# Kernel optimization log

Measured on AMD Instinct MI355X. Metric: run time of the kernel, lower is better.

Reference implementation:

```python
import jax, jax.numpy as jnp
import numpy as np

N, E, G = 50000, 800000, 64          # nodes, edges, graphs
IN, HID, OUT, H = 256, 64, 64, 4     # input dim, per-head hidden, output dim, heads
NEG_SLOPE = 0.2                      # PyG GATConv leaky_relu slope


def _lin(k, fan_in, fan_out):
    return jax.random.normal(k, (fan_in, fan_out), jnp.float32) * (1.0 / np.sqrt(fan_in))


def setup_inputs() -> dict:
    key = jax.random.key(0)
    ks = jax.random.split(key, 16)
    x = jax.random.normal(ks[0], (N, IN), jnp.float32)
    edge_index = jax.random.randint(ks[1], (2, E), 0, N, dtype=jnp.int32)
    batch = jnp.sort(jax.random.randint(ks[2], (N,), 0, G, dtype=jnp.int32))
    # layer 1: IN -> H x HID (concat)
    W1 = _lin(ks[3], IN, H * HID)
    a_src1 = jax.random.normal(ks[4], (H, HID), jnp.float32) * 0.1
    a_dst1 = jax.random.normal(ks[5], (H, HID), jnp.float32) * 0.1
    b1 = jnp.zeros((H * HID,), jnp.float32)
    # layer 2: H*HID -> H x HID (concat)
    W2 = _lin(ks[6], H * HID, H * HID)
    a_src2 = jax.random.normal(ks[7], (H, HID), jnp.float32) * 0.1
    a_dst2 = jax.random.normal(ks[8], (H, HID), jnp.float32) * 0.1
    b2 = jnp.zeros((H * HID,), jnp.float32)
    W3 = _lin(ks[9], H * HID, OUT)
    a_src3 = jax.random.normal(ks[10], (1, OUT), jnp.float32) * 0.1
    a_dst3 = jax.random.normal(ks[11], (1, OUT), jnp.float32) * 0.1
    b3 = jnp.zeros((OUT,), jnp.float32)
    return {"x": x, "edge_index": edge_index, "batch": batch,
            "W1": W1, "a_src1": a_src1, "a_dst1": a_dst1, "b1": b1,
            "W2": W2, "a_src2": a_src2, "a_dst2": a_dst2, "b2": b2,
            "W3": W3, "a_src3": a_src3, "a_dst3": a_dst3, "b3": b3}


def gat_conv(x, src, dst, W, a_src, a_dst, b, heads, out_ch):
    """PyG-style GATConv (eval mode, concat=True semantics; heads=1 == no concat)."""
    n = x.shape[0]
    h = (x @ W).reshape(n, heads, out_ch)                     # [N,H,C]
    alpha_s = jnp.sum(h * a_src, axis=-1)                     # [N,H]
    alpha_d = jnp.sum(h * a_dst, axis=-1)                     # [N,H]
    e = jax.nn.leaky_relu(alpha_s[src] + alpha_d[dst], NEG_SLOPE)  # [E',H]
    # segment softmax over destination nodes (self-loops guarantee nonempty segments)
    m = jax.ops.segment_max(e, dst, num_segments=n)
    e = jnp.exp(e - m[dst])
    denom = jax.ops.segment_sum(e, dst, num_segments=n)
    alpha = e / (denom[dst] + 1e-16)                          # [E',H]
    msg = h[src] * alpha[:, :, None]                          # [E',H,C]
    out = jax.ops.segment_sum(msg, dst, num_segments=n)       # [N,H,C]
    return out.reshape(n, heads * out_ch) + b


def reference(x, edge_index, batch, W1, a_src1, a_dst1, b1, W2, a_src2, a_dst2, b2,
              W3, a_src3, a_dst3, b3):
    n = x.shape[0]
    # GATConv default add_self_loops=True
    loops = jnp.arange(n, dtype=edge_index.dtype)
    src = jnp.concatenate([edge_index[0], loops])
    dst = jnp.concatenate([edge_index[1], loops])

    h = gat_conv(x, src, dst, W1, a_src1, a_dst1, b1, H, HID)
    h = jax.nn.elu(h)  # dropout disabled in eval
    h = gat_conv(h, src, dst, W2, a_src2, a_dst2, b2, H, HID)
    h = jax.nn.elu(h)
    node_embeddings = gat_conv(h, src, dst, W3, a_src3, a_dst3, b3, 1, OUT)

    # global_mean_pool over batch ids
    sums = jax.ops.segment_sum(node_embeddings, batch, num_segments=G)
    counts = jax.ops.segment_sum(jnp.ones((n,), node_embeddings.dtype), batch, num_segments=G)
    graph_embeddings = sums / jnp.maximum(counts, 1.0)[:, None]
    return node_embeddings, graph_embeddings
```

## Files before the change

kernel.cpp:

```cpp
#include <hip/hip_runtime.h>
#include <hip/hip_bf16.h>
#include <hip/hip_fp16.h>

typedef __attribute__((ext_vector_type(8))) _Float16 f16x8;
typedef __attribute__((ext_vector_type(4))) _Float16 f16x4;
typedef __attribute__((ext_vector_type(4))) float f32x4;

static __device__ __forceinline__ void st(float* p, float v)  { *p = v; }
static __device__ __forceinline__ void st(__half* p, float v) { *p = __float2half(v); }

static __device__ __forceinline__ void splitf16(float v, __half& hi, __half& lo) {
    hi = __float2half(v);
    lo = __float2half(v - __half2float(hi));
}

__global__ void k_pre(const int* __restrict__ ei, int* __restrict__ deg, int* __restrict__ rnk,
                      int E,
                      const float* __restrict__ x, __half* __restrict__ xh,
                      __half* __restrict__ xl, long n4,
                      const float* __restrict__ W1, const float* __restrict__ W2,
                      const float* __restrict__ W3,
                      __half* __restrict__ w1h, __half* __restrict__ w1l,
                      __half* __restrict__ w2h, __half* __restrict__ w2l,
                      __half* __restrict__ w3h, __half* __restrict__ w3l) {
    int bx = blockIdx.x;
    int nhist = (E + 255) >> 8;
    if (bx < nhist) {
        int e = bx * 256 + threadIdx.x;
        if (e < E) rnk[e] = atomicAdd(&deg[ei[E + e]], 1);
        return;
    }
    bx -= nhist;
    int nx4 = (int)((n4 + 255) >> 8);
    if (bx < nx4) {
        long i = (long)bx * 256 + threadIdx.x;
        if (i < n4) {
            float4 v = *reinterpret_cast<const float4*>(x + i * 4);
            __half h0, h1, h2, h3, l0, l1, l2, l3;
            splitf16(v.x, h0, l0);
            splitf16(v.y, h1, l1);
            splitf16(v.z, h2, l2);
            splitf16(v.w, h3, l3);
            ushort4 hv = { __half_as_ushort(h0), __half_as_ushort(h1),
                           __half_as_ushort(h2), __half_as_ushort(h3) };
            ushort4 lv = { __half_as_ushort(l0), __half_as_ushort(l1),
                           __half_as_ushort(l2), __half_as_ushort(l3) };
            *reinterpret_cast<ushort4*>(xh + i * 4) = hv;
            *reinterpret_cast<ushort4*>(xl + i * 4) = lv;
        }
        return;
    }
    bx -= nx4;
    int idx = bx * 256 + threadIdx.x;
    const float* W; __half *Wh, *Wl; int M, base;
    constexpr int K = 256;
    if (idx < 65536)       { W = W1; Wh = w1h; Wl = w1l; M = 256; base = idx; }
    else if (idx < 131072) { W = W2; Wh = w2h; Wl = w2l; M = 256; base = idx - 65536; }
    else if (idx < 147456) { W = W3; Wh = w3h; Wl = w3l; M = 64;  base = idx - 131072; }
    else return;
    int k = base / M, n = base - k * M;
    __half h, l;
    splitf16(W[base], h, l);
    Wh[(size_t)n * K + k] = h;
    Wl[(size_t)n * K + k] = l;
}

__global__ void k_scan1(const int* __restrict__ deg, int* __restrict__ offs,
                        int* __restrict__ bsum, int N) {
    __shared__ int sh[256];
    int i = blockIdx.x * 256 + threadIdx.x;
    int v = (i < N) ? (deg[i] + 1) : 0;
    sh[threadIdx.x] = v;
    __syncthreads();
#pragma unroll
    for (int off = 1; off < 256; off <<= 1) {
        int t = (threadIdx.x >= off) ? sh[threadIdx.x - off] : 0;
        __syncthreads();
        sh[threadIdx.x] += t;
        __syncthreads();
    }
    if (i < N) offs[i] = sh[threadIdx.x] - v;
    if (threadIdx.x == 255) bsum[blockIdx.x] = sh[255];
}

__global__ void k_scan2(int* __restrict__ bsum, int nb) {
    __shared__ int sh[256];
    int v = (threadIdx.x < nb) ? bsum[threadIdx.x] : 0;
    sh[threadIdx.x] = v;
    __syncthreads();
#pragma unroll
    for (int off = 1; off < 256; off <<= 1) {
        int t = (threadIdx.x >= off) ? sh[threadIdx.x - off] : 0;
        __syncthreads();
        sh[threadIdx.x] += t;
        __syncthreads();
    }
    if (threadIdx.x < nb) bsum[threadIdx.x] = sh[threadIdx.x] - v;
    if (threadIdx.x == 255) bsum[nb] = sh[255];
}

__global__ void k_scan3(int* __restrict__ offs, const int* __restrict__ deg,
                        int* __restrict__ csr, const int* __restrict__ bsum,
                        int N, int nb) {
    int i = blockIdx.x * 256 + threadIdx.x;
    if (i < N) {
        int v = offs[i] + bsum[blockIdx.x];
        offs[i] = v;
        csr[v + deg[i]] = i;
    }
    if (i == 0) offs[N] = bsum[nb];
}

template <typename ACC>
static __device__ __forceinline__ void alpha_epilogue(
        const ACC& acc, float* ldsf, const float* __restrict__ a_src,
        const float* __restrict__ a_dst, float* __restrict__ als,
        float* __restrict__ ald, __half* __restrict__ C,
        int nrows, int M, int H, int r0, int c0,
        int wr, int wc, int quad, int r, int tid) {
    float ps[4][4], pd[4][4];
#pragma unroll
    for (int tr = 0; tr < 4; ++tr)
#pragma unroll
        for (int i = 0; i < 4; ++i) { ps[tr][i] = 0.f; pd[tr][i] = 0.f; }

#pragma unroll
    for (int tr = 0; tr < 4; ++tr)
#pragma unroll
        for (int tc = 0; tc < 2; ++tc) {
            int col = c0 + wc * 32 + tc * 16 + r;
            float av_s = a_src[col], av_d = a_dst[col];
#pragma unroll
            for (int i = 0; i < 4; ++i) {
                int row = r0 + wr * 64 + tr * 16 + quad * 4 + i;
                __half hv = __float2half(acc[tr][tc][i]);
                float vr = __half2float(hv);
                if (row < nrows) C[(size_t)row * M + col] = hv;
                ps[tr][i] = fmaf(vr, av_s, ps[tr][i]);
                pd[tr][i] = fmaf(vr, av_d, pd[tr][i]);
            }
        }
#pragma unroll
    for (int tr = 0; tr < 4; ++tr)
#pragma unroll
        for (int i = 0; i < 4; ++i) {
            float s = ps[tr][i], d2 = pd[tr][i];
#pragma unroll
            for (int off = 1; off < 16; off <<= 1) {
                s  += __shfl_xor(s,  off, 64);
                d2 += __shfl_xor(d2, off, 64);
            }
            if (r == 0) {
                int lrow = wr * 64 + tr * 16 + quad * 4 + i;
                ldsf[(0 * 2 + wc) * 128 + lrow] = s;
                ldsf[(2 + wc) * 128 + lrow]     = d2;
            }
        }
    __syncthreads();
    int lrow = tid >> 1, which = tid & 1;
    if (lrow < 128) {
        float v = ldsf[(which * 2 + 0) * 128 + lrow] + ldsf[(which * 2 + 1) * 128 + lrow];
        int grow = r0 + lrow;
        if (grow < nrows) {
            float* dst = which ? ald : als;
            dst[(size_t)grow * H + (c0 >> 6)] = v;
        }
    }
}

__global__ __launch_bounds__(256) void k_g3s(const __half* __restrict__ Ah, const __half* __restrict__ Al,
                                             const __half* __restrict__ Wth, const __half* __restrict__ Wtl,
                                             __half* __restrict__ C, int nrows, int K, int M,
                                             const float* __restrict__ a_src, const float* __restrict__ a_dst,
                                             float* __restrict__ als, float* __restrict__ ald, int H,
                                             int gridRows, int gemmBlocks,
                                             const int* __restrict__ ei, const int* __restrict__ rnk,
                                             const int* __restrict__ offs, int* __restrict__ csr, int E) {
    constexpr int LDA = 40;
    __shared__ __half AH[128 * LDA];
    __shared__ __half AL[128 * LDA];
    __shared__ __half BH[64 * LDA];
    __shared__ __half BL[64 * LDA];

    int gx = blockIdx.x;
    int g = gx / 3, rsel = gx - g * 3;
    if (rsel != 0) {
        int e = (g * 2 + (rsel - 1)) * 256 + threadIdx.x;
        if (e < E) {
            int dn = ei[E + e];
            csr[offs[dn] + rnk[e]] = ei[e];
        }
        return;
    }
    if (g >= gemmBlocks) return;
    int bxg = g % gridRows, byg = g / gridRows;

    int tid  = threadIdx.x;
    int lane = tid & 63;
    int wave = tid >> 6;
    int wr = wave & 1, wc = wave >> 1;
    int quad = lane >> 4, r = lane & 15;
    int r0 = bxg * 128, c0 = byg * 64;

    f32x4 acc[4][2];
#pragma unroll
    for (int i = 0; i < 4; ++i)
#pragma unroll
        for (int j = 0; j < 2; ++j) acc[i][j] = (f32x4){0.f, 0.f, 0.f, 0.f};

    for (int kc = 0; kc < K; kc += 32) {
#pragma unroll
        for (int it = 0; it < 2; ++it) {
            int row  = (tid >> 2) + it * 64;
            int kseg = (tid & 3) * 8;
            int gr = r0 + row;
            f16x8 vh = (f16x8)(_Float16)0, vl = (f16x8)(_Float16)0;
            if (gr < nrows) {
                vh = *reinterpret_cast<const f16x8*>(Ah + (size_t)gr * K + kc + kseg);
                vl = *reinterpret_cast<const f16x8*>(Al + (size_t)gr * K + kc + kseg);
            }
            *reinterpret_cast<f16x8*>(&AH[row * LDA + kseg]) = vh;
            *reinterpret_cast<f16x8*>(&AL[row * LDA + kseg]) = vl;
        }
        {
            int n    = tid >> 2;
            int kseg = (tid & 3) * 8;
            *reinterpret_cast<f16x8*>(&BH[n * LDA + kseg]) =
                *reinterpret_cast<const f16x8*>(Wth + (size_t)(c0 + n) * K + kc + kseg);
            *reinterpret_cast<f16x8*>(&BL[n * LDA + kseg]) =
                *reinterpret_cast<const f16x8*>(Wtl + (size_t)(c0 + n) * K + kc + kseg);
        }
        __syncthreads();
        int k0 = quad * 8;
        f16x8 ah[4], al[4], bh[2], bl[2];
#pragma unroll
        for (int tr = 0; tr < 4; ++tr) {
            int row = wr * 64 + tr * 16 + r;
            ah[tr] = *reinterpret_cast<const f16x8*>(&AH[row * LDA + k0]);
            al[tr] = *reinterpret_cast<const f16x8*>(&AL[row * LDA + k0]);
        }
#pragma unroll
        for (int tc = 0; tc < 2; ++tc) {
            int col = wc * 32 + tc * 16 + r;
            bh[tc] = *reinterpret_cast<const f16x8*>(&BH[col * LDA + k0]);
            bl[tc] = *reinterpret_cast<const f16x8*>(&BL[col * LDA + k0]);
        }
#pragma unroll
        for (int tr = 0; tr < 4; ++tr)
#pragma unroll
            for (int tc = 0; tc < 2; ++tc) {
                acc[tr][tc] = __builtin_amdgcn_mfma_f32_16x16x32_f16(ah[tr], bh[tc], acc[tr][tc], 0, 0, 0);
                acc[tr][tc] = __builtin_amdgcn_mfma_f32_16x16x32_f16(ah[tr], bl[tc], acc[tr][tc], 0, 0, 0);
                acc[tr][tc] = __builtin_amdgcn_mfma_f32_16x16x32_f16(al[tr], bh[tc], acc[tr][tc], 0, 0, 0);
            }
        __syncthreads();
    }
    alpha_epilogue(acc, reinterpret_cast<float*>(AH), a_src, a_dst, als, ald, C,
                   nrows, M, H, r0, c0, wr, wc, quad, r, tid);
}

__global__ __launch_bounds__(256) void k_gemm2(const __half* __restrict__ A,
                                               const __half* __restrict__ Wth, const __half* __restrict__ Wtl,
                                               __half* __restrict__ C, int nrows, int K, int M,
                                               const float* __restrict__ a_src, const float* __restrict__ a_dst,
                                               float* __restrict__ als, float* __restrict__ ald, int H) {
    constexpr int LDA = 40;
    __shared__ __half AS[128 * LDA];
    __shared__ __half BH[64 * LDA];
    __shared__ __half BL[64 * LDA];

    int tid  = threadIdx.x;
    int lane = tid & 63;
    int wave = tid >> 6;
    int wr = wave & 1, wc = wave >> 1;
    int quad = lane >> 4, r = lane & 15;
    int r0 = blockIdx.x * 128, c0 = blockIdx.y * 64;

    f32x4 acc[4][2];
#pragma unroll
    for (int i = 0; i < 4; ++i)
#pragma unroll
        for (int j = 0; j < 2; ++j) acc[i][j] = (f32x4){0.f, 0.f, 0.f, 0.f};

    for (int kc = 0; kc < K; kc += 32) {
#pragma unroll
        for (int it = 0; it < 2; ++it) {
            int row  = (tid >> 2) + it * 64;
            int kseg = (tid & 3) * 8;
            int gr = r0 + row;
            f16x8 v = (f16x8)(_Float16)0;
            if (gr < nrows) v = *reinterpret_cast<const f16x8*>(A + (size_t)gr * K + kc + kseg);
            *reinterpret_cast<f16x8*>(&AS[row * LDA + kseg]) = v;
        }
        {
            int n    = tid >> 2;
            int kseg = (tid & 3) * 8;
            *reinterpret_cast<f16x8*>(&BH[n * LDA + kseg]) =
                *reinterpret_cast<const f16x8*>(Wth + (size_t)(c0 + n) * K + kc + kseg);
            *reinterpret_cast<f16x8*>(&BL[n * LDA + kseg]) =
                *reinterpret_cast<const f16x8*>(Wtl + (size_t)(c0 + n) * K + kc + kseg);
        }
        __syncthreads();
        int k0 = quad * 8;
        f16x8 a[4], bh[2], bl[2];
#pragma unroll
        for (int tr = 0; tr < 4; ++tr) {
            int row = wr * 64 + tr * 16 + r;
            a[tr] = *reinterpret_cast<const f16x8*>(&AS[row * LDA + k0]);
        }
#pragma unroll
        for (int tc = 0; tc < 2; ++tc) {
            int col = wc * 32 + tc * 16 + r;
            bh[tc] = *reinterpret_cast<const f16x8*>(&BH[col * LDA + k0]);
            bl[tc] = *reinterpret_cast<const f16x8*>(&BL[col * LDA + k0]);
        }
#pragma unroll
        for (int tr = 0; tr < 4; ++tr)
#pragma unroll
            for (int tc = 0; tc < 2; ++tc) {
                acc[tr][tc] = __builtin_amdgcn_mfma_f32_16x16x32_f16(a[tr], bh[tc], acc[tr][tc], 0, 0, 0);
                acc[tr][tc] = __builtin_amdgcn_mfma_f32_16x16x32_f16(a[tr], bl[tc], acc[tr][tc], 0, 0, 0);
            }
        __syncthreads();
    }
    alpha_epilogue(acc, reinterpret_cast<float*>(AS), a_src, a_dst, als, ald, C,
                   nrows, M, H, r0, c0, wr, wc, quad, r, tid);
}

template <int CHUNK, bool ELU, typename OT>
__global__ void k_agg(const __half* __restrict__ feat, const int* __restrict__ offs,
                      const int* __restrict__ csr, const float* __restrict__ als,
                      const float* __restrict__ ald, const float* __restrict__ bias,
                      OT* __restrict__ out, int N) {
    constexpr int M  = 64 * CHUNK;
    constexpr int H  = (CHUNK == 4) ? 4 : 1;
    constexpr int EC = 16;
    constexpr int SH = (CHUNK == 4) ? 9 : 7;

    __shared__ float    shw[4][2][64];
    __shared__ unsigned sho[4][2][EC];

    int tid  = threadIdx.x;
    int lane = tid & 63;
    int wid  = tid >> 6;
    int node = blockIdx.x * 4 + wid;
    if (node >= N) return;

    int ia = lane & 15;
    int ha = (H == 4) ? (lane >> 4) : 0;
    int ho = lane >> 4;

    float adv = ald[(size_t)node * H + ha];

    int beg = offs[node], end = offs[node + 1];
    int d   = end - beg;
    int nc  = (d + EC - 1) >> 4;

    const char* fbase = reinterpret_cast<const char*>(feat) + lane * (CHUNK * 2);

    float acc[CHUNK] = {};
    float den = 0.f;

    int sv = csr[beg + min(ia, min(EC, d) - 1)];
    float xv = als[(size_t)sv * H + ha];
    int sv_n = sv;
    if (nc > 1) {
        int cn = min(EC, d - EC);
        sv_n = csr[beg + EC + min(ia, cn - 1)];
    }

    for (int c = 0; c < nc; ++c) {
        int cnt = min(EC, d - c * EC);

        float e = xv + adv;
        e = (e > 0.f) ? e : 0.2f * e;
        float w = (ia < cnt) ? __expf(e) : 0.f;
        den += w;
        int b = c & 1;
        shw[wid][b][lane] = w;
        if (lane < EC) sho[wid][b][lane] = (unsigned)sv << SH;

        xv = als[(size_t)sv_n * H + ha];
        sv = sv_n;
        if (c + 2 < nc) {
            int cn = min(EC, d - (c + 2) * EC);
            sv_n = csr[beg + (c + 2) * EC + min(ia, cn - 1)];
        }

        const float* wp = &shw[wid][b][ho * EC];
        float4 w0 = *reinterpret_cast<const float4*>(wp);
        float4 w1 = *reinterpret_cast<const float4*>(wp + 4);
        float4 w2 = *reinterpret_cast<const float4*>(wp + 8);
        float4 w3 = *reinterpret_cast<const float4*>(wp + 12);
        const unsigned* op = &sho[wid][b][0];
        uint4 o0 = *reinterpret_cast<const uint4*>(op);
        uint4 o1 = *reinterpret_cast<const uint4*>(op + 4);
        uint4 o2 = *reinterpret_cast<const uint4*>(op + 8);
        uint4 o3 = *reinterpret_cast<const uint4*>(op + 12);
        float    ww[EC] = {w0.x, w0.y, w0.z, w0.w, w1.x, w1.y, w1.z, w1.w,
                           w2.x, w2.y, w2.z, w2.w, w3.x, w3.y, w3.z, w3.w};
        unsigned oo[EC] = {o0.x, o0.y, o0.z, o0.w, o1.x, o1.y, o1.z, o1.w,
                           o2.x, o2.y, o2.z, o2.w, o3.x, o3.y, o3.z, o3.w};
        if constexpr (CHUNK == 4) {
            f16x4 v[EC];
#pragma unroll
            for (int t = 0; t < EC; ++t)
                v[t] = *reinterpret_cast<const f16x4*>(fbase + oo[t]);
#pragma unroll
            for (int t = 0; t < EC; ++t)
#pragma unroll
                for (int j = 0; j < 4; ++j)
                    acc[j] = fmaf((float)v[t][j], ww[t], acc[j]);
        } else {
            __half v[EC];
#pragma unroll
            for (int t = 0; t < EC; ++t)
                v[t] = *reinterpret_cast<const __half*>(fbase + oo[t]);
#pragma unroll
            for (int t = 0; t < EC; ++t)
                acc[0] = fmaf(__half2float(v[t]), ww[t], acc[0]);
        }
    }

#pragma unroll
    for (int off = 1; off < EC; off <<= 1) den += __shfl_xor(den, off, 64);
    float inv = 1.f / (den + 1e-16f);

#pragma unroll
    for (int j = 0; j < CHUNK; ++j) {
        int col = lane * CHUNK + j;
        float v = acc[j] * inv + bias[col];
        if (ELU) v = (v > 0.f) ? v : (__expf(v) - 1.f);
        st(&out[(size_t)node * M + col], v);
    }
}

static __device__ __forceinline__ int lowerb(const int* __restrict__ a, int n, int v) {
    int lo = 0, hi = n;
    while (lo < hi) { int mid = (lo + hi) >> 1; if (a[mid] < v) lo = mid + 1; else hi = mid; }
    return lo;
}

__global__ void k_pool2(const float* __restrict__ ne, const int* __restrict__ batch,
                        float* __restrict__ gout, int N) {
    int g = blockIdx.x;
    int lo = lowerb(batch, N, g);
    int hi = lowerb(batch, N, g + 1);
    int lane = threadIdx.x & 63, row = threadIdx.x >> 6;
    float s = 0.f;
    for (int i = lo + row; i < hi; i += 4) s += ne[(size_t)i * 64 + lane];
    __shared__ float red[4][64];
    red[row][lane] = s;
    __syncthreads();
    if (row == 0) {
        float v = red[0][lane] + red[1][lane] + red[2][lane] + red[3][lane];
        gout[(size_t)g * 64 + lane] = v / fmaxf((float)(hi - lo), 1.f);
    }
}

extern "C" void kernel_launch(void* const* d_in, const int* in_sizes, int n_in,
                              void* d_out, int out_size, void* d_ws, size_t ws_size,
                              hipStream_t stream) {
    const float* x   = (const float*)d_in[0];
    const int* ei    = (const int*)d_in[1];
    const int* batch = (const int*)d_in[2];
    const float* W1  = (const float*)d_in[3];
    const float* as1 = (const float*)d_in[4];
    const float* ad1 = (const float*)d_in[5];
    const float* b1  = (const float*)d_in[6];
    const float* W2  = (const float*)d_in[7];
    const float* as2 = (const float*)d_in[8];
    const float* ad2 = (const float*)d_in[9];
    const float* b2  = (const float*)d_in[10];
    const float* W3  = (const float*)d_in[11];
    const float* as3 = (const float*)d_in[12];
    const float* ad3 = (const float*)d_in[13];
    const float* b3  = (const float*)d_in[14];

    const int N = in_sizes[2];
    const int E = in_sizes[1] / 2;
    const int G = 64;
    float* out = (float*)d_out;

    char* w = (char*)d_ws;
    auto carve = [&](size_t bytes) { char* p = w; w += (bytes + 255) & ~(size_t)255; return p; };
    __half* feat = (__half*)carve((size_t)N * 256 * 2);
    __half* xh   = (__half*)carve((size_t)N * 256 * 2);
    __half* xl   = (__half*)carve((size_t)N * 256 * 2);
    __half* act  = xh;
    float* als   = (float*)carve((size_t)N * 4 * 4);
    float* ald   = (float*)carve((size_t)N * 4 * 4);
    int* deg     = (int*)carve((size_t)N * 4);
    int* offs    = (int*)carve((size_t)(N + 1) * 4);
    int* rnk     = (int*)carve((size_t)E * 4);
    int* csr     = (int*)carve((size_t)(E + N) * 4);
    int nb       = (N + 255) / 256;
    int* bsum    = (int*)carve((size_t)(nb + 1) * 4);
    __half* w1h  = (__half*)carve((size_t)256 * 256 * 2);
    __half* w1l  = (__half*)carve((size_t)256 * 256 * 2);
    __half* w2h  = (__half*)carve((size_t)256 * 256 * 2);
    __half* w2l  = (__half*)carve((size_t)256 * 256 * 2);
    __half* w3h  = (__half*)carve((size_t)256 * 64 * 2);
    __half* w3l  = (__half*)carve((size_t)256 * 64 * 2);

    long n4 = (long)N * 64;
    int nhist = (E + 255) / 256;
    int nx4   = (int)((n4 + 255) / 256);
    int nwspl = (147456 + 255) / 256;

    hipMemsetAsync(deg, 0, (size_t)N * 4, stream);
    k_pre<<<nhist + nx4 + nwspl, 256, 0, stream>>>(ei, deg, rnk, E, x, xh, xl, n4,
                                                   W1, W2, W3, w1h, w1l, w2h, w2l, w3h, w3l);

    k_scan1<<<nb, 256, 0, stream>>>(deg, offs, bsum, N);
    k_scan2<<<1, 256, 0, stream>>>(bsum, nb);
    k_scan3<<<nb, 256, 0, stream>>>(offs, deg, csr, bsum, N, nb);

    int gridRows = (N + 127) / 128;
    int gemmBlocks = gridRows * 4;
    int nodeBlocks = (N + 3) / 4;

    k_g3s<<<3 * gemmBlocks, 256, 0, stream>>>(xh, xl, w1h, w1l, feat, N, 256, 256,
                                              as1, ad1, als, ald, 4,
                                              gridRows, gemmBlocks, ei, rnk, offs, csr, E);
    k_agg<4, true, __half><<<nodeBlocks, 256, 0, stream>>>(feat, offs, csr, als, ald, b1, act, N);
    k_gemm2<<<dim3(gridRows, 4), 256, 0, stream>>>(act, w2h, w2l, feat, N, 256, 256,
                                                   as2, ad2, als, ald, 4);
    k_agg<4, true, __half><<<nodeBlocks, 256, 0, stream>>>(feat, offs, csr, als, ald, b2, act, N);
    k_gemm2<<<dim3(gridRows, 1), 256, 0, stream>>>(act, w3h, w3l, feat, N, 256, 64,
                                                   as3, ad3, als, ald, 1);
    k_agg<1, false, float><<<nodeBlocks, 256, 0, stream>>>(feat, offs, csr, als, ald, b3, out, N);

    k_pool2<<<G, 256, 0, stream>>>(out, batch, out + (size_t)N * 64, N);
}
```

Measured before the change: 497.1 us.

## Widen layer-1/2 GEMM tiles to 128x128 with per-wave head alpha epilogue

The split-fp16 GEMMs for layers 1 and 2 now use 128x128 output tiles instead of 128x64, so each wave covers a full 64-column head. This halves the number of column blocks and halves how often the A tile is re-read from global memory. Because each wave owns a whole head, the attention-logit reduction is done with in-wave shuffles instead of an LDS-staged cross-wave sum. The fused CSR-scatter blocks in the layer-1 kernel are rebalanced to four per GEMM block to keep the same edge coverage. The cost is roughly double the accumulator registers and larger LDS per block, which may reduce occupancy.

Result: faster. 475.5 us (-4.4%).

```diff
diff --git a/kernel.cpp b/kernel.cpp
--- a/kernel.cpp
+++ b/kernel.cpp
@@ -168,31 +168,78 @@
     }
 }
 
+template <typename ACC>
+static __device__ __forceinline__ void alpha_epilogue_w(
+        const ACC& acc, const float* __restrict__ a_src, const float* __restrict__ a_dst,
+        float* __restrict__ als, float* __restrict__ ald, __half* __restrict__ C,
+        int nrows, int M, int H, int r0, int c0, int wr, int wc, int quad, int r) {
+    int head = (c0 >> 6) + wc;
+    float ps[4][4], pd[4][4];
+#pragma unroll
+    for (int tr = 0; tr < 4; ++tr)
+#pragma unroll
+        for (int i = 0; i < 4; ++i) { ps[tr][i] = 0.f; pd[tr][i] = 0.f; }
+
+#pragma unroll
+    for (int tr = 0; tr < 4; ++tr)
+#pragma unroll
+        for (int tc = 0; tc < 4; ++tc) {
+            int col = c0 + wc * 64 + tc * 16 + r;
+            float av_s = a_src[col], av_d = a_dst[col];
+#pragma unroll
+            for (int i = 0; i < 4; ++i) {
+                int row = r0 + wr * 64 + tr * 16 + quad * 4 + i;
+                __half hv = __float2half(acc[tr][tc][i]);
+                float vr = __half2float(hv);
+                if (row < nrows) C[(size_t)row * M + col] = hv;
+                ps[tr][i] = fmaf(vr, av_s, ps[tr][i]);
+                pd[tr][i] = fmaf(vr, av_d, pd[tr][i]);
+            }
+        }
+#pragma unroll
+    for (int tr = 0; tr < 4; ++tr)
+#pragma unroll
+        for (int i = 0; i < 4; ++i) {
+            float s = ps[tr][i], d2 = pd[tr][i];
+#pragma unroll
+            for (int off = 1; off < 16; off <<= 1) {
+                s  += __shfl_xor(s,  off, 64);
+                d2 += __shfl_xor(d2, off, 64);
+            }
+            if (r == 0) {
+                int row = r0 + wr * 64 + tr * 16 + quad * 4 + i;
+                if (row < nrows) {
+                    als[(size_t)row * H + head] = s;
+                    ald[(size_t)row * H + head] = d2;
+                }
+            }
+        }
+}
+
 __global__ __launch_bounds__(256) void k_g3s(const __half* __restrict__ Ah, const __half* __restrict__ Al,
                                              const __half* __restrict__ Wth, const __half* __restrict__ Wtl,
                                              __half* __restrict__ C, int nrows, int K, int M,
                                              const float* __restrict__ a_src, const float* __restrict__ a_dst,
                                              float* __restrict__ als, float* __restrict__ ald, int H,
-                                             int gridRows, int gemmBlocks,
+                                             int gridRows,
                                              const int* __restrict__ ei, const int* __restrict__ rnk,
                                              const int* __restrict__ offs, int* __restrict__ csr, int E) {
     constexpr int LDA = 40;
     __shared__ __half AH[128 * LDA];
     __shared__ __half AL[128 * LDA];
-    __shared__ __half BH[64 * LDA];
-    __shared__ __half BL[64 * LDA];
+    __shared__ __half BH[128 * LDA];
+    __shared__ __half BL[128 * LDA];
 
     int gx = blockIdx.x;
-    int g = gx / 3, rsel = gx - g * 3;
+    int g = gx / 5, rsel = gx - g * 5;
     if (rsel != 0) {
-        int e = (g * 2 + (rsel - 1)) * 256 + threadIdx.x;
+        int e = (g * 4 + (rsel - 1)) * 256 + threadIdx.x;
         if (e < E) {
             int dn = ei[E + e];
             csr[offs[dn] + rnk[e]] = ei[e];
         }
         return;
     }
-    if (g >= gemmBlocks) return;
     int bxg = g % gridRows, byg = g / gridRows;
 
     int tid  = threadIdx.x;
@@ -200,13 +247,13 @@
     int wave = tid >> 6;
     int wr = wave & 1, wc = wave >> 1;
     int quad = lane >> 4, r = lane & 15;
-    int r0 = bxg * 128, c0 = byg * 64;
-
-    f32x4 acc[4][2];
+    int r0 = bxg * 128, c0 = byg * 128;
+
+    f32x4 acc[4][4];
 #pragma unroll
     for (int i = 0; i < 4; ++i)
 #pragma unroll
-        for (int j = 0; j < 2; ++j) acc[i][j] = (f32x4){0.f, 0.f, 0.f, 0.f};
+        for (int j = 0; j < 4; ++j) acc[i][j] = (f32x4){0.f, 0.f, 0.f, 0.f};
 
     for (int kc = 0; kc < K; kc += 32) {
 #pragma unroll
@@ -222,8 +269,9 @@
             *reinterpret_cast<f16x8*>(&AH[row * LDA + kseg]) = vh;
             *reinterpret_cast<f16x8*>(&AL[row * LDA + kseg]) = vl;
         }
-        {
-            int n    = tid >> 2;
+#pragma unroll
+        for (int it = 0; it < 2; ++it) {
+            int n    = (tid >> 2) + it * 64;
             int kseg = (tid & 3) * 8;
             *reinterpret_cast<f16x8*>(&BH[n * LDA + kseg]) =
                 *reinterpret_cast<const f16x8*>(Wth + (size_t)(c0 + n) * K + kc + kseg);
@@ -232,7 +280,7 @@
         }
         __syncthreads();
         int k0 = quad * 8;
-        f16x8 ah[4], al[4], bh[2], bl[2];
+        f16x8 ah[4], al[4], bh[4], bl[4];
 #pragma unroll
         for (int tr = 0; tr < 4; ++tr) {
             int row = wr * 64 + tr * 16 + r;
@@ -240,23 +288,90 @@
             al[tr] = *reinterpret_cast<const f16x8*>(&AL[row * LDA + k0]);
         }
 #pragma unroll
-        for (int tc = 0; tc < 2; ++tc) {
-            int col = wc * 32 + tc * 16 + r;
+        for (int tc = 0; tc < 4; ++tc) {
+            int col = wc * 64 + tc * 16 + r;
             bh[tc] = *reinterpret_cast<const f16x8*>(&BH[col * LDA + k0]);
             bl[tc] = *reinterpret_cast<const f16x8*>(&BL[col * LDA + k0]);
         }
 #pragma unroll
         for (int tr = 0; tr < 4; ++tr)
 #pragma unroll
-            for (int tc = 0; tc < 2; ++tc) {
+            for (int tc = 0; tc < 4; ++tc) {
                 acc[tr][tc] = __builtin_amdgcn_mfma_f32_16x16x32_f16(ah[tr], bh[tc], acc[tr][tc], 0, 0, 0);
                 acc[tr][tc] = __builtin_amdgcn_mfma_f32_16x16x32_f16(ah[tr], bl[tc], acc[tr][tc], 0, 0, 0);
                 acc[tr][tc] = __builtin_amdgcn_mfma_f32_16x16x32_f16(al[tr], bh[tc], acc[tr][tc], 0, 0, 0);
             }
         __syncthreads();
     }
-    alpha_epilogue(acc, reinterpret_cast<float*>(AH), a_src, a_dst, als, ald, C,
-                   nrows, M, H, r0, c0, wr, wc, quad, r, tid);
+    alpha_epilogue_w(acc, a_src, a_dst, als, ald, C, nrows, M, H, r0, c0, wr, wc, quad, r);
+}
+
+__global__ __launch_bounds__(256) void k_gemm2w(const __half* __restrict__ A,
+                                                const __half* __restrict__ Wth, const __half* __restrict__ Wtl,
+                                                __half* __restrict__ C, int nrows, int K, int M,
+                                                const float* __restrict__ a_src, const float* __restrict__ a_dst,
+                                                float* __restrict__ als, float* __restrict__ ald, int H) {
+    constexpr int LDA = 40;
+    __shared__ __half AS[128 * LDA];
+    __shared__ __half BH[128 * LDA];
+    __shared__ __half BL[128 * LDA];
+
+    int tid  = threadIdx.x;
+    int lane = tid & 63;
+    int wave = tid >> 6;
+    int wr = wave & 1, wc = wave >> 1;
+    int quad = lane >> 4, r = lane & 15;
+    int r0 = blockIdx.x * 128, c0 = blockIdx.y * 128;
+
+    f32x4 acc[4][4];
+#pragma unroll
+    for (int i = 0; i < 4; ++i)
+#pragma unroll
+        for (int j = 0; j < 4; ++j) acc[i][j] = (f32x4){0.f, 0.f, 0.f, 0.f};
+
+    for (int kc = 0; kc < K; kc += 32) {
+#pragma unroll
+        for (int it = 0; it < 2; ++it) {
+            int row  = (tid >> 2) + it * 64;
+            int kseg = (tid & 3) * 8;
+            int gr = r0 + row;
+            f16x8 v = (f16x8)(_Float16)0;
+            if (gr < nrows) v = *reinterpret_cast<const f16x8*>(A + (size_t)gr * K + kc + kseg);
+            *reinterpret_cast<f16x8*>(&AS[row * LDA + kseg]) = v;
+        }
+#pragma unroll
+        for (int it = 0; it < 2; ++it) {
+            int n    = (tid >> 2) + it * 64;
+            int kseg = (tid & 3) * 8;
+            *reinterpret_cast<f16x8*>(&BH[n * LDA + kseg]) =
+                *reinterpret_cast<const f16x8*>(Wth + (size_t)(c0 + n) * K + kc + kseg);
+            *reinterpret_cast<f16x8*>(&BL[n * LDA + kseg]) =
+                *reinterpret_cast<const f16x8*>(Wtl + (size_t)(c0 + n) * K + kc + kseg);
+        }
+        __syncthreads();
+        int k0 = quad * 8;
+        f16x8 a[4], bh[4], bl[4];
+#pragma unroll
+        for (int tr = 0; tr < 4; ++tr) {
+            int row = wr * 64 + tr * 16 + r;
+            a[tr] = *reinterpret_cast<const f16x8*>(&AS[row * LDA + k0]);
+        }
+#pragma unroll
+        for (int tc = 0; tc < 4; ++tc) {
+            int col = wc * 64 + tc * 16 + r;
+            bh[tc] = *reinterpret_cast<const f16x8*>(&BH[col * LDA + k0]);
+            bl[tc] = *reinterpret_cast<const f16x8*>(&BL[col * LDA + k0]);
+        }
+#pragma unroll
+        for (int tr = 0; tr < 4; ++tr)
+#pragma unroll
+            for (int tc = 0; tc < 4; ++tc) {
+                acc[tr][tc] = __builtin_amdgcn_mfma_f32_16x16x32_f16(a[tr], bh[tc], acc[tr][tc], 0, 0, 0);
+                acc[tr][tc] = __builtin_amdgcn_mfma_f32_16x16x32_f16(a[tr], bl[tc], acc[tr][tc], 0, 0, 0);
+            }
+        __syncthreads();
+    }
+    alpha_epilogue_w(acc, a_src, a_dst, als, ald, C, nrows, M, H, r0, c0, wr, wc, quad, r);
 }
 
 __global__ __launch_bounds__(256) void k_gemm2(const __half* __restrict__ A,
@@ -517,15 +632,15 @@
     k_scan3<<<nb, 256, 0, stream>>>(offs, deg, csr, bsum, N, nb);
 
     int gridRows = (N + 127) / 128;
-    int gemmBlocks = gridRows * 4;
+    int gemmBlocks = gridRows * 2;
     int nodeBlocks = (N + 3) / 4;
 
-    k_g3s<<<3 * gemmBlocks, 256, 0, stream>>>(xh, xl, w1h, w1l, feat, N, 256, 256,
+    k_g3s<<<5 * gemmBlocks, 256, 0, stream>>>(xh, xl, w1h, w1l, feat, N, 256, 256,
                                               as1, ad1, als, ald, 4,
-                                              gridRows, gemmBlocks, ei, rnk, offs, csr, E);
+                                              gridRows, ei, rnk, offs, csr, E);
     k_agg<4, true, __half><<<nodeBlocks, 256, 0, stream>>>(feat, offs, csr, als, ald, b1, act, N);
-    k_gemm2<<<dim3(gridRows, 4), 256, 0, stream>>>(act, w2h, w2l, feat, N, 256, 256,
-                                                   as2, ad2, als, ald, 4);
+    k_gemm2w<<<dim3(gridRows, 2), 256, 0, stream>>>(act, w2h, w2l, feat, N, 256, 256,
+                                                    as2, ad2, als, ald, 4);
     k_agg<4, true, __half><<<nodeBlocks, 256, 0, stream>>>(feat, offs, csr, als, ald, b2, act, N);
     k_gemm2<<<dim3(gridRows, 1), 256, 0, stream>>>(act, w3h, w3l, feat, N, 256, 64,
                                                    as3, ad3, als, ald, 1);
```
